# Performance work log

Measured on AMD Instinct MI355X. Metric: run time of the kernel, lower is better.

## Reference

```python
import jax, jax.numpy as jnp
import numpy as np

B, N, E = 256, 50000, 128000


def setup_inputs() -> dict:
    key = jax.random.key(0)
    ks = jax.random.split(key, 12)
    # forward args (normalized predictions / demand truth)
    pred_p_norm = jax.random.normal(ks[0], (B, N), dtype=jnp.float32)
    pred_f_norm = jax.random.normal(ks[1], (B, E), dtype=jnp.float32)
    true_d_norm = jax.random.normal(ks[2], (B, N), dtype=jnp.float32)
    # scaler params (positive scales)
    p_mean = jax.random.normal(ks[3], (N,), dtype=jnp.float32) * 10.0 + 50.0
    p_scale = jax.random.uniform(ks[4], (N,), dtype=jnp.float32, minval=0.5, maxval=5.0)
    f_mean = jax.random.normal(ks[5], (E,), dtype=jnp.float32) * 0.1
    f_scale = jax.random.uniform(ks[6], (E,), dtype=jnp.float32, minval=0.01, maxval=1.0)
    d_mean = jax.random.normal(ks[7], (N,), dtype=jnp.float32) * 0.01
    d_scale = jax.random.uniform(ks[8], (N,), dtype=jnp.float32, minval=0.001, maxval=0.1)
    node_elevation = jax.random.uniform(ks[9], (N,), dtype=jnp.float32, minval=0.0, maxval=300.0)
    # edge static attrs -> Hazen-Williams resistance R = 10.67 * L * (C+eps)^-1.852 * (D+eps)^-4.87
    L = jax.random.uniform(ks[10], (E,), dtype=jnp.float32, minval=10.0, maxval=1000.0)
    D = jax.random.uniform(ks[11], (E,), dtype=jnp.float32, minval=0.05, maxval=1.0)
    C = jnp.full((E,), 130.0, dtype=jnp.float32)
    eps = 1e-06
    R = 10.67 * L * (C + eps) ** (-1.852) * (D + eps) ** (-4.87)
    edge_index = jax.random.randint(jax.random.fold_in(key, 99), (2, E), 0, N, dtype=jnp.int32)
    return {
        'pred_p_norm': pred_p_norm, 'pred_f_norm': pred_f_norm, 'true_d_norm': true_d_norm,
        'p_mean': p_mean, 'p_scale': p_scale, 'f_mean': f_mean, 'f_scale': f_scale,
        'd_mean': d_mean, 'd_scale': d_scale, 'node_elevation': node_elevation,
        'R': R, 'edge_index': edge_index,
    }


def reference(pred_p_norm, pred_f_norm, true_d_norm, p_mean, p_scale, f_mean, f_scale,
              d_mean, d_scale, node_elevation, R, edge_index):
    n_nodes = pred_p_norm.shape[1]
    # denormalize (broadcast per-node / per-edge scalers over batch)
    P = pred_p_norm * p_scale[None, :] + p_mean[None, :]          # [B, N]
    Q = pred_f_norm * f_scale[None, :] + f_mean[None, :]          # [B, E]
    d = true_d_norm * d_scale[None, :] + d_mean[None, :]          # [B, N]
    H = P + node_elevation[None, :]                               # hydraulic head [B, N]
    src, dst = edge_index[0], edge_index[1]
    # mass conservation: net inflow per node vs demand
    Q_T = Q.T                                                      # [E, B]
    q_out = jax.ops.segment_sum(Q_T, src, num_segments=n_nodes).T  # [B, N]
    q_in = jax.ops.segment_sum(Q_T, dst, num_segments=n_nodes).T   # [B, N]
    q_net = q_in - q_out
    loss_mass = jnp.mean((q_net - d) ** 2)
    # head loss (Hazen-Williams): delta_h vs R*Q*|Q|^0.852
    h_src = H[:, src]                                              # [B, E]
    h_dst = H[:, dst]                                              # [B, E]
    delta_h_pred = h_src - h_dst
    friction_slope = R[None, :] * Q * jnp.abs(Q) ** 0.852
    loss_head = jnp.mean((delta_h_pred - friction_slope) ** 2)
    return (loss_mass, loss_head)
```

## Files before the change

kernel.cpp:

```cpp
#include <hip/hip_runtime.h>
#include <hip/hip_fp16.h>

#define TILE 64

__global__ void k_build_ht(const float* __restrict__ pred_p,
                           const float* __restrict__ p_scale,
                           const float* __restrict__ p_mean,
                           const float* __restrict__ elev,
                           const float* __restrict__ true_d,
                           const float* __restrict__ d_scale,
                           const float* __restrict__ d_mean,
                           const int* __restrict__ nodes,
                           int* __restrict__ deg,
                           int M,
                           __half* __restrict__ HTh,
                           __half* __restrict__ TD,
                           int B, int N) {
    __shared__ __align__(16) float tile[TILE][TILE + 2];
    const int n0 = blockIdx.x * TILE;
    const int b0 = blockIdx.y * TILE;
    const int tn = threadIdx.x % TILE;
    const int tw = threadIdx.x / TILE;
    const int c  = threadIdx.x & 31;
    const int rg = threadIdx.x >> 5;
    const int n = n0 + tn;

    const int flat = blockIdx.y * gridDim.x + blockIdx.x;
    if (flat < (M + 255) / 256) {
        const int i = flat * 256 + threadIdx.x;
        if (i < M) atomicAdd(&deg[nodes[i]], 1);
    }

    {
        float sc = 0.f, mn = 0.f, el = 0.f;
        if (n < N) { sc = p_scale[n]; mn = p_mean[n]; el = elev[n]; }
        #pragma unroll
        for (int i = 0; i < TILE / 4; ++i) {
            const int bl = i * 4 + tw;
            float v = 0.f;
            if (n < N) v = pred_p[(size_t)(b0 + bl) * N + n] * sc + mn + el;
            tile[tn][bl] = v;
        }
        __syncthreads();
        #pragma unroll
        for (int i = 0; i < 8; ++i) {
            const int nl = i * 8 + rg;
            const int nn = n0 + nl;
            if (nn < N) {
                const float2 f = *reinterpret_cast<const float2*>(&tile[nl][2 * c]);
                reinterpret_cast<__half2*>(HTh + (size_t)nn * B + b0)[c] =
                    __floats2half2_rn(f.x, f.y);
            }
        }
    }
    __syncthreads();
    {
        float sc = 0.f, mn = 0.f;
        if (n < N) { sc = d_scale[n]; mn = d_mean[n]; }
        #pragma unroll
        for (int i = 0; i < TILE / 4; ++i) {
            const int bl = i * 4 + tw;
            float v = 0.f;
            if (n < N) v = true_d[(size_t)(b0 + bl) * N + n] * sc + mn;
            tile[tn][bl] = v;
        }
        __syncthreads();
        #pragma unroll
        for (int i = 0; i < 8; ++i) {
            const int nl = i * 8 + rg;
            const int nn = n0 + nl;
            if (nn < N) {
                const float2 f = *reinterpret_cast<const float2*>(&tile[nl][2 * c]);
                reinterpret_cast<__half2*>(TD + (size_t)nn * B + b0)[c] =
                    __floats2half2_rn(f.x, f.y);
            }
        }
    }
}

__global__ void k_scan1(const int* __restrict__ deg, int* __restrict__ bsum, int N) {
    __shared__ int s[256];
    const int i = blockIdx.x * 256 + threadIdx.x;
    s[threadIdx.x] = (i < N) ? deg[i] : 0;
    __syncthreads();
    #pragma unroll
    for (int off = 128; off >= 1; off >>= 1) {
        if (threadIdx.x < off) s[threadIdx.x] += s[threadIdx.x + off];
        __syncthreads();
    }
    if (threadIdx.x == 0) bsum[blockIdx.x] = s[0];
}

__global__ void k_scan2(int* __restrict__ bsum, int nb) {
    __shared__ int s[256];
    const int t = threadIdx.x;
    const int v = (t < nb) ? bsum[t] : 0;
    s[t] = v;
    __syncthreads();
    #pragma unroll
    for (int off = 1; off < 256; off <<= 1) {
        const int tmp = (t >= off) ? s[t - off] : 0;
        __syncthreads();
        s[t] += tmp;
        __syncthreads();
    }
    if (t < nb) bsum[t] = s[t] - v;
}

__global__ void k_scan3(const int* __restrict__ deg, const int* __restrict__ bsum,
                        int* __restrict__ offsets, int* __restrict__ cursor, int N) {
    __shared__ int s[256];
    const int t = threadIdx.x;
    const int i = blockIdx.x * 256 + t;
    const int v = (i < N) ? deg[i] : 0;
    s[t] = v;
    __syncthreads();
    #pragma unroll
    for (int off = 1; off < 256; off <<= 1) {
        const int tmp = (t >= off) ? s[t - off] : 0;
        __syncthreads();
        s[t] += tmp;
        __syncthreads();
    }
    const int excl = s[t] - v + bsum[blockIdx.x];
    if (i < N) { offsets[i] = excl; cursor[i] = excl; }
    if (i == N - 1) offsets[N] = excl + v;
}

__global__ void k_fill(const int* __restrict__ esrc, const int* __restrict__ edst,
                       int* __restrict__ cursor, int* __restrict__ inc, int E) {
    const int e = blockIdx.x * 256 + threadIdx.x;
    if (e < E) {
        const int ps = atomicAdd(&cursor[esrc[e]], 1);
        inc[ps] = (e << 1);
        const int pd = atomicAdd(&cursor[edst[e]], 1);
        inc[pd] = (e << 1) | 1;
    }
}

__global__ __launch_bounds__(256) void k_edges(
        const float* __restrict__ pred_f,
        const float* __restrict__ f_scale,
        const float* __restrict__ f_mean,
        const float* __restrict__ Rcoef,
        const int* __restrict__ esrc,
        const int* __restrict__ edst,
        const __half* __restrict__ HTh,
        __half* __restrict__ QT,
        double* __restrict__ headp,
        int E) {
    __shared__ __align__(16) __half qth[TILE][258];
    __shared__ double wsum[4];
    const int e0 = blockIdx.x * TILE;
    const int tn = threadIdx.x & 63;
    const int tw = threadIdx.x >> 6;

    const int e = e0 + tn;
    const float fs = f_scale[e];
    const float fm = f_mean[e];

    #pragma unroll
    for (int sb = 0; sb < 4; ++sb) {
        #pragma unroll
        for (int i = 0; i < 16; ++i) {
            const int bl = i * 4 + tw;
            const float v = pred_f[(size_t)(sb * 64 + bl) * E + e] * fs + fm;
            qth[tn][sb * 64 + bl] = __float2half_rn(v);
        }
    }
    __syncthreads();

    uint2 hsv[16], hdv[16];
    float Rv[16];
    #pragma unroll
    for (int j = 0; j < 16; ++j) {
        const int el = tw * 16 + j;
        const int ee = e0 + el;
        const int s = esrc[ee];
        const int d = edst[ee];
        Rv[j] = Rcoef[ee];
        hsv[j] = *reinterpret_cast<const uint2*>(
            (const char*)HTh + (size_t)s * 512 + (size_t)tn * 8);
        hdv[j] = *reinterpret_cast<const uint2*>(
            (const char*)HTh + (size_t)d * 512 + (size_t)tn * 8);
        const uint2 q4 = *reinterpret_cast<const uint2*>(
            (const char*)&qth[el][0] + (size_t)tn * 8);
        *reinterpret_cast<uint2*>(
            (char*)QT + (size_t)ee * 512 + (size_t)tn * 8) = q4;
    }

    double head = 0.0;
    #pragma unroll
    for (int j = 0; j < 16; ++j) {
        const int el = tw * 16 + j;
        const uint2 q4 = *reinterpret_cast<const uint2*>(
            (const char*)&qth[el][0] + (size_t)tn * 8);
        const __half2 qa = *reinterpret_cast<const __half2*>(&q4.x);
        const __half2 qb = *reinterpret_cast<const __half2*>(&q4.y);
        const __half2 sa = *reinterpret_cast<const __half2*>(&hsv[j].x);
        const __half2 sb2 = *reinterpret_cast<const __half2*>(&hsv[j].y);
        const __half2 da = *reinterpret_cast<const __half2*>(&hdv[j].x);
        const __half2 db = *reinterpret_cast<const __half2*>(&hdv[j].y);
        const float2 qf0 = __half22float2(qa), qf1 = __half22float2(qb);
        const float2 sf0 = __half22float2(sa), sf1 = __half22float2(sb2);
        const float2 df0 = __half22float2(da), df1 = __half22float2(db);
        const float R = Rv[j];

        float qv[4] = {qf0.x, qf0.y, qf1.x, qf1.y};
        float sv[4] = {sf0.x, sf0.y, sf1.x, sf1.y};
        float dv[4] = {df0.x, df0.y, df1.x, df1.y};
        #pragma unroll
        for (int r = 0; r < 4; ++r) {
            const float q = qv[r];
            const float aq = fabsf(q);
            const float pw = exp2f(0.852f * __log2f(aq));
            const float fr = R * q * pw;
            const float t = (sv[r] - dv[r]) - fr;
            head += (double)t * (double)t;
        }
    }

    #pragma unroll
    for (int off = 32; off >= 1; off >>= 1)
        head += __shfl_down(head, off, 64);
    if ((threadIdx.x & 63) == 0) wsum[threadIdx.x >> 6] = head;
    __syncthreads();
    if (threadIdx.x == 0)
        headp[blockIdx.x] = wsum[0] + wsum[1] + wsum[2] + wsum[3];
}

__global__ __launch_bounds__(256) void k_nodemass(
        const __half* __restrict__ QT,
        const __half* __restrict__ TD,
        const int* __restrict__ offsets,
        const int* __restrict__ inc,
        double* __restrict__ massp,
        int N) {
    __shared__ double wsum[4];
    const int w = threadIdx.x >> 6;
    const int lane = threadIdx.x & 63;
    const int n = blockIdx.x * 4 + w;

    double m = 0.0;
    if (n < N) {
        const uint2 tdr = *reinterpret_cast<const uint2*>(
            (const char*)TD + (size_t)n * 512 + (size_t)lane * 8);

        const int beg = offsets[n];
        const int end = offsets[n + 1];
        const int cnt = end - beg;

        float qn0 = 0.f, qn1 = 0.f, qn2 = 0.f, qn3 = 0.f;
        if (cnt <= 4) {
            int   ivv[4];
            float sg[4];
            uint2 vv[4];
            #pragma unroll
            for (int u = 0; u < 4; ++u) {
                const int kk = (beg + u < end) ? (beg + u) : (end - 1);
                ivv[u] = inc[kk];
                sg[u] = (beg + u < end) ? ((ivv[u] & 1) ? 1.f : -1.f) : 0.f;
                vv[u] = *reinterpret_cast<const uint2*>(
                    (const char*)QT + (size_t)(ivv[u] >> 1) * 512
                                    + (size_t)lane * 8);
            }
            #pragma unroll
            for (int u = 0; u < 4; ++u) {
                const __half2 a = *reinterpret_cast<const __half2*>(&vv[u].x);
                const __half2 b = *reinterpret_cast<const __half2*>(&vv[u].y);
                const float2 fa = __half22float2(a);
                const float2 fb = __half22float2(b);
                qn0 += sg[u] * fa.x; qn1 += sg[u] * fa.y;
                qn2 += sg[u] * fb.x; qn3 += sg[u] * fb.y;
            }
        } else {
            for (int k = beg; k < end; k += 8) {
                int   ivv[8];
                float sg[8];
                uint2 vv[8];
                #pragma unroll
                for (int u = 0; u < 8; ++u) {
                    const int kk = (k + u < end) ? (k + u) : (end - 1);
                    ivv[u] = inc[kk];
                    sg[u] = (k + u < end) ? ((ivv[u] & 1) ? 1.f : -1.f) : 0.f;
                    vv[u] = *reinterpret_cast<const uint2*>(
                        (const char*)QT + (size_t)(ivv[u] >> 1) * 512
                                        + (size_t)lane * 8);
                }
                #pragma unroll
                for (int u = 0; u < 8; ++u) {
                    const __half2 a = *reinterpret_cast<const __half2*>(&vv[u].x);
                    const __half2 b = *reinterpret_cast<const __half2*>(&vv[u].y);
                    const float2 fa = __half22float2(a);
                    const float2 fb = __half22float2(b);
                    qn0 += sg[u] * fa.x; qn1 += sg[u] * fa.y;
                    qn2 += sg[u] * fb.x; qn3 += sg[u] * fb.y;
                }
            }
        }

        const __half2 d01 = *reinterpret_cast<const __half2*>(&tdr.x);
        const __half2 d23 = *reinterpret_cast<const __half2*>(&tdr.y);
        const float2 f01 = __half22float2(d01);
        const float2 f23 = __half22float2(d23);
        const float t0 = qn0 - f01.x;
        const float t1 = qn1 - f01.y;
        const float t2 = qn2 - f23.x;
        const float t3 = qn3 - f23.y;
        m = (double)t0 * t0 + (double)t1 * t1
          + (double)t2 * t2 + (double)t3 * t3;
    }

    #pragma unroll
    for (int off = 32; off >= 1; off >>= 1)
        m += __shfl_down(m, off, 64);
    if (lane == 0) wsum[w] = m;
    __syncthreads();
    if (threadIdx.x == 0)
        massp[blockIdx.x] = wsum[0] + wsum[1] + wsum[2] + wsum[3];
}

__global__ void k_reduce(const double* __restrict__ massp, int nm,
                         const double* __restrict__ headp, int nh,
                         float* __restrict__ out,
                         double inv_mass, double inv_head) {
    __shared__ double sh[256];
    const int t = threadIdx.x;

    double s = 0.0;
    for (int i = t; i < nm; i += 256) s += massp[i];
    sh[t] = s;
    __syncthreads();
    #pragma unroll
    for (int off = 128; off >= 1; off >>= 1) {
        if (t < off) sh[t] += sh[t + off];
        __syncthreads();
    }
    double mass_total = 0.0;
    if (t == 0) mass_total = sh[0];
    __syncthreads();

    s = 0.0;
    for (int i = t; i < nh; i += 256) s += headp[i];
    sh[t] = s;
    __syncthreads();
    #pragma unroll
    for (int off = 128; off >= 1; off >>= 1) {
        if (t < off) sh[t] += sh[t + off];
        __syncthreads();
    }
    if (t == 0) {
        out[0] = (float)(mass_total * inv_mass);
        out[1] = (float)(sh[0] * inv_head);
    }
}

static inline size_t align256s(size_t x) { return (x + 255) & ~(size_t)255; }

extern "C" void kernel_launch(void* const* d_in, const int* in_sizes, int n_in,
                              void* d_out, int out_size, void* d_ws, size_t ws_size,
                              hipStream_t stream) {
    const float* pred_p  = (const float*)d_in[0];
    const float* pred_f  = (const float*)d_in[1];
    const float* true_d  = (const float*)d_in[2];
    const float* p_mean  = (const float*)d_in[3];
    const float* p_scale = (const float*)d_in[4];
    const float* f_mean  = (const float*)d_in[5];
    const float* f_scale = (const float*)d_in[6];
    const float* d_mean  = (const float*)d_in[7];
    const float* d_scale = (const float*)d_in[8];
    const float* elev    = (const float*)d_in[9];
    const float* Rcoef   = (const float*)d_in[10];
    const int*   eidx    = (const int*)d_in[11];

    const int N = in_sizes[3];
    const int E = in_sizes[10];
    const int B = in_sizes[0] / N;

    const int* esrc = eidx;
    const int* edst = eidx + E;

    const int gn = (N + TILE - 1) / TILE;
    const int gb = B / TILE;
    const int ge = E / TILE;
    const int nbk = (N + 255) / 256;
    const int nmB = (N + 3) / 4;

    char* ws = (char*)d_ws;
    size_t off = 0;
    __half* HTh   = (__half*)(ws + off); off = align256s(off + (size_t)N * B * 2);
    __half* TD    = (__half*)(ws + off); off = align256s(off + (size_t)N * B * 2);
    __half* QT    = (__half*)(ws + off); off = align256s(off + (size_t)E * B * 2);
    int* incarr   = (int*)(ws + off);    off = align256s(off + (size_t)2 * E * 4);
    int* offsets  = (int*)(ws + off);    off = align256s(off + (size_t)(N + 1) * 4);
    int* cursor   = (int*)(ws + off);    off = align256s(off + (size_t)N * 4);
    double* headp = (double*)(ws + off); off = align256s(off + (size_t)ge * 8);
    double* massp = (double*)(ws + off); off = align256s(off + (size_t)nmB * 8);
    const size_t zero_beg = off;
    int* deg      = (int*)(ws + off);    off = align256s(off + (size_t)N * 4);
    int* bsum     = (int*)(ws + off);    off = align256s(off + 256 * 4);
    const size_t zero_len = off - zero_beg;

    hipMemsetAsync(ws + zero_beg, 0, zero_len, stream);

    k_build_ht<<<dim3(gn, gb), 256, 0, stream>>>(pred_p, p_scale, p_mean, elev,
                                                 true_d, d_scale, d_mean,
                                                 eidx, deg, 2 * E,
                                                 HTh, TD, B, N);
    k_scan1<<<nbk, 256, 0, stream>>>(deg, bsum, N);
    k_scan2<<<1, 256, 0, stream>>>(bsum, nbk);
    k_scan3<<<nbk, 256, 0, stream>>>(deg, bsum, offsets, cursor, N);
    k_fill <<<(E + 255) / 256, 256, 0, stream>>>(esrc, edst, cursor, incarr, E);

    k_edges<<<ge, 256, 0, stream>>>(pred_f, f_scale, f_mean, Rcoef,
                                    esrc, edst, HTh, QT, headp, E);
    k_nodemass<<<nmB, 256, 0, stream>>>(QT, TD, offsets, incarr, massp, N);
    k_reduce<<<1, 256, 0, stream>>>(massp, nmB, headp, ge,
                                    (float*)d_out,
                                    1.0 / ((double)B * (double)N),
                                    1.0 / ((double)B * (double)E));
}
```

Before: 175.8 us.

## Split edge kernel over batch tiles with a 2D grid

The edge kernel now launches a 2D grid over (edge tile, 64-wide batch tile) instead of one block handling all 256 batch columns per edge tile. Each block uses a much smaller shared tile and fewer registers, which gives more blocks and higher occupancy. The cost is 2-byte scalar half loads from the gathered head rows instead of 8-byte vector loads. It also rereads the edge indices and R once per batch tile and needs four times as many partial sums in the final reduction.

```diff
diff --git a/kernel.cpp b/kernel.cpp
--- a/kernel.cpp
+++ b/kernel.cpp
@@ -148,10 +148,11 @@
         const __half* __restrict__ HTh,
         __half* __restrict__ QT,
         double* __restrict__ headp,
-        int E) {
-    __shared__ __align__(16) __half qth[TILE][258];
+        int B, int E) {
+    __shared__ __align__(16) __half qth[TILE][66];
     __shared__ double wsum[4];
     const int e0 = blockIdx.x * TILE;
+    const int b0 = blockIdx.y * TILE;
     const int tn = threadIdx.x & 63;
     const int tw = threadIdx.x >> 6;
 
@@ -160,64 +161,44 @@
     const float fm = f_mean[e];
 
     #pragma unroll
-    for (int sb = 0; sb < 4; ++sb) {
-        #pragma unroll
-        for (int i = 0; i < 16; ++i) {
-            const int bl = i * 4 + tw;
-            const float v = pred_f[(size_t)(sb * 64 + bl) * E + e] * fs + fm;
-            qth[tn][sb * 64 + bl] = __float2half_rn(v);
-        }
-    }
-    __syncthreads();
-
-    uint2 hsv[16], hdv[16];
-    float Rv[16];
+    for (int i = 0; i < 16; ++i) {
+        const int bl = i * 4 + tw;
+        const float v = pred_f[(size_t)(b0 + bl) * E + e] * fs + fm;
+        qth[tn][bl] = __float2half_rn(v);
+    }
+    __syncthreads();
+
+    float hs[16], hd[16], Rv[16];
     #pragma unroll
     for (int j = 0; j < 16; ++j) {
-        const int el = tw * 16 + j;
-        const int ee = e0 + el;
+        const int ee = e0 + tw * 16 + j;
         const int s = esrc[ee];
         const int d = edst[ee];
         Rv[j] = Rcoef[ee];
-        hsv[j] = *reinterpret_cast<const uint2*>(
-            (const char*)HTh + (size_t)s * 512 + (size_t)tn * 8);
-        hdv[j] = *reinterpret_cast<const uint2*>(
-            (const char*)HTh + (size_t)d * 512 + (size_t)tn * 8);
-        const uint2 q4 = *reinterpret_cast<const uint2*>(
-            (const char*)&qth[el][0] + (size_t)tn * 8);
-        *reinterpret_cast<uint2*>(
-            (char*)QT + (size_t)ee * 512 + (size_t)tn * 8) = q4;
+        hs[j] = __half2float(HTh[(size_t)s * 256 + b0 + tn]);
+        hd[j] = __half2float(HTh[(size_t)d * 256 + b0 + tn]);
+    }
+
+    const int sel = tn >> 5;
+    const int pc  = tn & 31;
+    #pragma unroll
+    for (int k = 0; k < 8; ++k) {
+        const int el = tw * 16 + 2 * k + sel;
+        const int ee = e0 + el;
+        const __half2 h = *reinterpret_cast<const __half2*>(&qth[el][2 * pc]);
+        *reinterpret_cast<__half2*>(QT + (size_t)ee * 256 + b0 + 2 * pc) = h;
     }
 
     double head = 0.0;
     #pragma unroll
     for (int j = 0; j < 16; ++j) {
         const int el = tw * 16 + j;
-        const uint2 q4 = *reinterpret_cast<const uint2*>(
-            (const char*)&qth[el][0] + (size_t)tn * 8);
-        const __half2 qa = *reinterpret_cast<const __half2*>(&q4.x);
-        const __half2 qb = *reinterpret_cast<const __half2*>(&q4.y);
-        const __half2 sa = *reinterpret_cast<const __half2*>(&hsv[j].x);
-        const __half2 sb2 = *reinterpret_cast<const __half2*>(&hsv[j].y);
-        const __half2 da = *reinterpret_cast<const __half2*>(&hdv[j].x);
-        const __half2 db = *reinterpret_cast<const __half2*>(&hdv[j].y);
-        const float2 qf0 = __half22float2(qa), qf1 = __half22float2(qb);
-        const float2 sf0 = __half22float2(sa), sf1 = __half22float2(sb2);
-        const float2 df0 = __half22float2(da), df1 = __half22float2(db);
-        const float R = Rv[j];
-
-        float qv[4] = {qf0.x, qf0.y, qf1.x, qf1.y};
-        float sv[4] = {sf0.x, sf0.y, sf1.x, sf1.y};
-        float dv[4] = {df0.x, df0.y, df1.x, df1.y};
-        #pragma unroll
-        for (int r = 0; r < 4; ++r) {
-            const float q = qv[r];
-            const float aq = fabsf(q);
-            const float pw = exp2f(0.852f * __log2f(aq));
-            const float fr = R * q * pw;
-            const float t = (sv[r] - dv[r]) - fr;
-            head += (double)t * (double)t;
-        }
+        const float q = __half2float(qth[el][tn]);
+        const float aq = fabsf(q);
+        const float pw = exp2f(0.852f * __log2f(aq));
+        const float fr = Rv[j] * q * pw;
+        const float t = (hs[j] - hd[j]) - fr;
+        head += (double)t * (double)t;
     }
 
     #pragma unroll
@@ -226,7 +207,8 @@
     if ((threadIdx.x & 63) == 0) wsum[threadIdx.x >> 6] = head;
     __syncthreads();
     if (threadIdx.x == 0)
-        headp[blockIdx.x] = wsum[0] + wsum[1] + wsum[2] + wsum[3];
+        headp[(size_t)blockIdx.y * gridDim.x + blockIdx.x] =
+            wsum[0] + wsum[1] + wsum[2] + wsum[3];
 }
 
 __global__ __launch_bounds__(256) void k_nodemass(
@@ -394,7 +376,7 @@
     int* incarr   = (int*)(ws + off);    off = align256s(off + (size_t)2 * E * 4);
     int* offsets  = (int*)(ws + off);    off = align256s(off + (size_t)(N + 1) * 4);
     int* cursor   = (int*)(ws + off);    off = align256s(off + (size_t)N * 4);
-    double* headp = (double*)(ws + off); off = align256s(off + (size_t)ge * 8);
+    double* headp = (double*)(ws + off); off = align256s(off + (size_t)ge * gb * 8);
     double* massp = (double*)(ws + off); off = align256s(off + (size_t)nmB * 8);
     const size_t zero_beg = off;
     int* deg      = (int*)(ws + off);    off = align256s(off + (size_t)N * 4);
@@ -412,10 +394,10 @@
     k_scan3<<<nbk, 256, 0, stream>>>(deg, bsum, offsets, cursor, N);
     k_fill <<<(E + 255) / 256, 256, 0, stream>>>(esrc, edst, cursor, incarr, E);
 
-    k_edges<<<ge, 256, 0, stream>>>(pred_f, f_scale, f_mean, Rcoef,
-                                    esrc, edst, HTh, QT, headp, E);
+    k_edges<<<dim3(ge, gb), 256, 0, stream>>>(pred_f, f_scale, f_mean, Rcoef,
+                                              esrc, edst, HTh, QT, headp, B, E);
     k_nodemass<<<nmB, 256, 0, stream>>>(QT, TD, offsets, incarr, massp, N);
-    k_reduce<<<1, 256, 0, stream>>>(massp, nmB, headp, ge,
+    k_reduce<<<1, 256, 0, stream>>>(massp, nmB, headp, ge * gb,
                                     (float*)d_out,
                                     1.0 / ((double)B * (double)N),
                                     1.0 / ((double)B * (double)E));
```

Result: no change. 179.3 us (+2.0%).
